# Performance work log

Hardware: AMD Instinct MI355X
Metric: run time of the kernel (lower is better)

Reference implementation:

```python
import math
import jax, jax.numpy as jnp
import numpy as np

L, D, H, DF, V, T, B = 4, 1024, 16, 4096, 32000, 2048, 1
HD = D // H
EPS = 1e-5

def _ln(x, w, b):
    m = jnp.mean(x, -1, keepdims=True)
    v = jnp.mean((x - m) ** 2, -1, keepdims=True)
    return (x - m) * jax.lax.rsqrt(v + EPS) * w + b

def setup_inputs() -> dict:
    key = jax.random.key(0)
    ks = jax.random.split(key, 8)
    s = 0.02
    return {
        'ids':   jax.random.randint(ks[0], (B, T), 0, V),
        'te':    jax.random.normal(ks[1], (V, D), jnp.float32) * s,
        'pe':    jax.random.normal(ks[2], (T, D), jnp.float32) * s,
        'qkv_w': jax.random.normal(ks[3], (L, D, 3 * D), jnp.float32) * s,
        'qkv_b': jnp.zeros((L, 3 * D), jnp.float32),
        'out_w': jax.random.normal(ks[4], (L, D, D), jnp.float32) * s,
        'out_b': jnp.zeros((L, D), jnp.float32),
        'ln1_w': jnp.ones((L, D), jnp.float32),
        'ln1_b': jnp.zeros((L, D), jnp.float32),
        'ln2_w': jnp.ones((L, D), jnp.float32),
        'ln2_b': jnp.zeros((L, D), jnp.float32),
        'up_w':  jax.random.normal(ks[5], (L, D, DF), jnp.float32) * s,
        'up_b':  jnp.zeros((L, DF), jnp.float32),
        'dn_w':  jax.random.normal(ks[6], (L, DF, D), jnp.float32) * s,
        'dn_b':  jnp.zeros((L, D), jnp.float32),
        'lnf_w': jnp.ones((D,), jnp.float32),
        'lnf_b': jnp.zeros((D,), jnp.float32),
    }

def reference(ids, te, pe, qkv_w, qkv_b, out_w, out_b, ln1_w, ln1_b,
              ln2_w, ln2_b, up_w, up_b, dn_w, dn_b, lnf_w, lnf_b):
    b, t = ids.shape
    x = te[ids] + pe[:t][None]                        # [b,t,D]
    causal = jnp.tril(jnp.ones((t, t), bool))          # [t,t]
    scale = 1.0 / math.sqrt(HD)
    for i in range(L):
        h = _ln(x, ln1_w[i], ln1_b[i])
        qkv = (h @ qkv_w[i] + qkv_b[i]).reshape(b, t, 3, H, HD)
        q, k, v = qkv[:, :, 0], qkv[:, :, 1], qkv[:, :, 2]
        sc = jnp.einsum('bqhd,bkhd->bhqk', q, k) * scale
        sc = jnp.where(causal, sc, -jnp.inf)
        att = jax.nn.softmax(sc, axis=-1)
        ao = jnp.einsum('bhqk,bkhd->bqhd', att, v).reshape(b, t, D)
        x = x + ao @ out_w[i] + out_b[i]
        h = _ln(x, ln2_w[i], ln2_b[i])
        x = x + jax.nn.silu(h @ up_w[i] + up_b[i]) @ dn_w[i] + dn_b[i]
    x = _ln(x, lnf_w, lnf_b)
    logits = x @ te.T                                  # tied head, no bias
    return logits
```

## Files before the change

### kernel.cpp

```cpp
#include <hip/hip_runtime.h>

typedef __attribute__((ext_vector_type(8))) short short8;
typedef __attribute__((ext_vector_type(4))) short short4v;
typedef __attribute__((ext_vector_type(4))) float f32x4;
typedef unsigned short u16;

#define Lc 4
#define Dc 1024
#define Hc 16
#define HDc 64
#define DFc 4096
#define Vc 32000
#define Tc 2048

__device__ __forceinline__ u16 f2bf(float f) {
  union { float f; unsigned u; } v; v.f = f;
  return (u16)((v.u + 0x7FFFu + ((v.u >> 16) & 1u)) >> 16);
}

__device__ __forceinline__ void gload_lds16(const u16* g, u16* l) {
  __builtin_amdgcn_global_load_lds(
      (const __attribute__((address_space(1))) unsigned int*)(g),
      (__attribute__((address_space(3))) unsigned int*)(l), 16, 0, 0);
}

#define BARS do { __builtin_amdgcn_s_barrier(); __builtin_amdgcn_sched_barrier(0); } while (0)
#define LGKM0 do { asm volatile("s_waitcnt lgkmcnt(0)" ::: "memory"); __builtin_amdgcn_sched_barrier(0); } while (0)
#define VMC(n) do { asm volatile("s_waitcnt vmcnt(" #n ")" ::: "memory"); __builtin_amdgcn_sched_barrier(0); } while (0)

__global__ __launch_bounds__(256) void castk(const float* __restrict__ in, u16* __restrict__ out) {
  size_t i = ((size_t)blockIdx.x * 256 + threadIdx.x) * 4;
  float4 v = *(const float4*)(in + i);
  short4v o; o[0] = f2bf(v.x); o[1] = f2bf(v.y); o[2] = f2bf(v.z); o[3] = f2bf(v.w);
  *(short4v*)(out + i) = o;
}

__global__ __launch_bounds__(256) void embedln(const int* __restrict__ ids, const float* __restrict__ te,
                                               const float* __restrict__ pe, const float* __restrict__ w,
                                               const float* __restrict__ b, float* __restrict__ x,
                                               u16* __restrict__ out) {
  int t = blockIdx.x, tid = threadIdx.x;
  int id = ids[t];
  float4 a = *(const float4*)(te + (size_t)id * Dc + tid * 4);
  float4 p = *(const float4*)(pe + (size_t)t * Dc + tid * 4);
  float4 v; v.x = a.x + p.x; v.y = a.y + p.y; v.z = a.z + p.z; v.w = a.w + p.w;
  size_t i = (size_t)t * Dc + tid * 4;
  *(float4*)(x + i) = v;
  float s = v.x + v.y + v.z + v.w;
  float q = v.x * v.x + v.y * v.y + v.z * v.z + v.w * v.w;
  #pragma unroll
  for (int off = 1; off < 64; off <<= 1) { s += __shfl_xor(s, off); q += __shfl_xor(q, off); }
  __shared__ float red[8];
  if ((tid & 63) == 0) { red[tid >> 6] = s; red[4 + (tid >> 6)] = q; }
  __syncthreads();
  s = red[0] + red[1] + red[2] + red[3];
  q = red[4] + red[5] + red[6] + red[7];
  float mean = s * (1.0f / Dc);
  float rstd = rsqrtf(q * (1.0f / Dc) - mean * mean + 1e-5f);
  float4 wv = *(const float4*)(w + tid * 4);
  float4 bv = *(const float4*)(b + tid * 4);
  out[i + 0] = f2bf((v.x - mean) * rstd * wv.x + bv.x);
  out[i + 1] = f2bf((v.y - mean) * rstd * wv.y + bv.y);
  out[i + 2] = f2bf((v.z - mean) * rstd * wv.z + bv.z);
  out[i + 3] = f2bf((v.w - mean) * rstd * wv.w + bv.w);
}

template<int SK>
__global__ __launch_bounds__(256) void combineln(float* __restrict__ x, const float* __restrict__ p,
                                                 const float* __restrict__ bias, const float* __restrict__ w,
                                                 const float* __restrict__ b, u16* __restrict__ out) {
  int t = blockIdx.x, tid = threadIdx.x;
  size_t i = (size_t)t * Dc + tid * 4;
  float4 v = *(const float4*)(x + i);
  #pragma unroll
  for (int s = 0; s < SK; s++) {
    float4 q2 = *(const float4*)(p + (size_t)s * Tc * Dc + i);
    v.x += q2.x; v.y += q2.y; v.z += q2.z; v.w += q2.w;
  }
  float4 bb = *(const float4*)(bias + tid * 4);
  v.x += bb.x; v.y += bb.y; v.z += bb.z; v.w += bb.w;
  *(float4*)(x + i) = v;
  float s = v.x + v.y + v.z + v.w;
  float q = v.x * v.x + v.y * v.y + v.z * v.z + v.w * v.w;
  #pragma unroll
  for (int off = 1; off < 64; off <<= 1) { s += __shfl_xor(s, off); q += __shfl_xor(q, off); }
  __shared__ float red[8];
  if ((tid & 63) == 0) { red[tid >> 6] = s; red[4 + (tid >> 6)] = q; }
  __syncthreads();
  s = red[0] + red[1] + red[2] + red[3];
  q = red[4] + red[5] + red[6] + red[7];
  float mean = s * (1.0f / Dc);
  float rstd = rsqrtf(q * (1.0f / Dc) - mean * mean + 1e-5f);
  float4 wv = *(const float4*)(w + tid * 4);
  float4 bv = *(const float4*)(b + tid * 4);
  out[i + 0] = f2bf((v.x - mean) * rstd * wv.x + bv.x);
  out[i + 1] = f2bf((v.y - mean) * rstd * wv.y + bv.y);
  out[i + 2] = f2bf((v.z - mean) * rstd * wv.z + bv.z);
  out[i + 3] = f2bf((v.w - mean) * rstd * wv.w + bv.w);
}

__global__ __launch_bounds__(256) void transpose4(const float* __restrict__ qw, const float* __restrict__ ow,
                                                  const float* __restrict__ uw, const float* __restrict__ dw,
                                                  u16* __restrict__ qT, u16* __restrict__ oT,
                                                  u16* __restrict__ uT, u16* __restrict__ dT) {
  __shared__ float tl[32][33];
  int id = blockIdx.x;
  const float* in; u16* out; int R, C, t;
  if (id < 3072)      { in = qw; out = qT; R = Dc;  C = 3 * Dc; t = id; }
  else if (id < 4096) { in = ow; out = oT; R = Dc;  C = Dc;     t = id - 3072; }
  else if (id < 8192) { in = uw; out = uT; R = Dc;  C = DFc;    t = id - 4096; }
  else                { in = dw; out = dT; R = DFc; C = Dc;     t = id - 8192; }
  int tilesX = C >> 5;
  int c0 = (t % tilesX) * 32, r0 = (t / tilesX) * 32;
  int lx = threadIdx.x & 31, ly = threadIdx.x >> 5;
  #pragma unroll
  for (int i = ly; i < 32; i += 8) tl[i][lx] = in[(size_t)(r0 + i) * C + c0 + lx];
  __syncthreads();
  #pragma unroll
  for (int i = ly; i < 32; i += 8) out[(size_t)(c0 + i) * R + r0 + lx] = f2bf(tl[lx][i]);
}

template<int EPI>
__global__ __launch_bounds__(256) void gemm128p(
    const u16* __restrict__ A, const u16* __restrict__ Bt, const float* __restrict__ bias,
    u16* __restrict__ outb, float* __restrict__ outf, int M, int N, int K, int KS) {
  __shared__ __align__(16) u16 lds[32768];
  u16* As = lds;
  u16* Bs = lds + 16384;
  const int NK = KS >> 6;

  int tid = threadIdx.x;
  int w = tid >> 6, lane = tid & 63;
  int lr = lane & 15, lg = lane >> 4;
  int wr = w >> 1, wc = w & 1;

  int m0 = blockIdx.y * 128, n0 = blockIdx.x * 128;
  int kbase = blockIdx.z * KS;

  int offg[4];
  #pragma unroll
  for (int j = 0; j < 4; j++) {
    int p = tid + j * 256;
    int row = p >> 3;
    int uc = (p & 7) ^ (row & 7);
    offg[j] = row * K + uc * 8;
  }
  const u16* aB = A + (size_t)m0 * K + kbase;
  const u16* bB = Bt + (size_t)n0 * K + kbase;

  auto stA = [&](int kt, int part) {
    u16* l = As + ((kt & 1) << 13) + w * 512;
    #pragma unroll
    for (int j = 2 * part; j < 2 * part + 2; j++)
      gload_lds16(aB + kt * 64 + offg[j], l + j * 2048);
  };
  auto stB = [&](int kt, int part) {
    u16* l = Bs + ((kt & 1) << 13) + w * 512;
    #pragma unroll
    for (int j = 2 * part; j < 2 * part + 2; j++)
      gload_lds16(bB + kt * 64 + offg[j], l + j * 2048);
  };

  int colx0 = ((0 * 4 + lg) ^ (lr & 7)) * 8;
  int colx1 = ((1 * 4 + lg) ^ (lr & 7)) * 8;
  int abase = (wr * 64 + lr) * 64;
  int bbase = (wc * 64 + lr) * 64;

  f32x4 acc[4][4] = {};

  stB(0, 0); stB(0, 1); stA(0, 0); stA(0, 1); stB(1, 0); stB(1, 1);
  VMC(4);
  BARS;

  for (int kt = 0; kt < NK; ++kt) {
    const u16* sA = As + ((kt & 1) << 13);
    const u16* sB = Bs + ((kt & 1) << 13);
    short8 af[4][2], bf[4][2];

    #pragma unroll
    for (int m = 0; m < 2; m++) {
      af[m][0] = *(const short8*)(sA + abase + m * 1024 + colx0);
      af[m][1] = *(const short8*)(sA + abase + m * 1024 + colx1);
      bf[m][0] = *(const short8*)(sB + bbase + m * 1024 + colx0);
      bf[m][1] = *(const short8*)(sB + bbase + m * 1024 + colx1);
    }
    if (kt + 1 < NK) stA(kt + 1, 0);
    BARS;
    LGKM0;
    __builtin_amdgcn_s_setprio(1);
    #pragma unroll
    for (int m = 0; m < 2; m++)
      #pragma unroll
      for (int n = 0; n < 2; n++)
        #pragma unroll
        for (int ks = 0; ks < 2; ks++)
          acc[m][n] = __builtin_amdgcn_mfma_f32_16x16x32_bf16(af[m][ks], bf[n][ks], acc[m][n], 0, 0, 0);
    __builtin_amdgcn_s_setprio(0);
    BARS;

    #pragma unroll
    for (int n = 2; n < 4; n++) {
      bf[n][0] = *(const short8*)(sB + bbase + n * 1024 + colx0);
      bf[n][1] = *(const short8*)(sB + bbase + n * 1024 + colx1);
    }
    if (kt + 1 < NK) stA(kt + 1, 1);
    BARS;
    LGKM0;
    __builtin_amdgcn_s_setprio(1);
    #pragma unroll
    for (int m = 0; m < 2; m++)
      #pragma unroll
      for (int n = 2; n < 4; n++)
        #pragma unroll
        for (int ks = 0; ks < 2; ks++)
          acc[m][n] = __builtin_amdgcn_mfma_f32_16x16x32_bf16(af[m][ks], bf[n][ks], acc[m][n], 0, 0, 0);
    __builtin_amdgcn_s_setprio(0);
    BARS;

    #pragma unroll
    for (int m = 2; m < 4; m++) {
      af[m][0] = *(const short8*)(sA + abase + m * 1024 + colx0);
      af[m][1] = *(const short8*)(sA + abase + m * 1024 + colx1);
    }
    if (kt + 2 < NK) stB(kt + 2, 0);
    BARS;
    LGKM0;
    __builtin_amdgcn_s_setprio(1);
    #pragma unroll
    for (int m = 2; m < 4; m++)
      #pragma unroll
      for (int n = 0; n < 2; n++)
        #pragma unroll
        for (int ks = 0; ks < 2; ks++)
          acc[m][n] = __builtin_amdgcn_mfma_f32_16x16x32_bf16(af[m][ks], bf[n][ks], acc[m][n], 0, 0, 0);
    __builtin_amdgcn_s_setprio(0);
    BARS;

    if (kt + 2 < NK) { stB(kt + 2, 1); VMC(4); }
    else if (kt + 1 < NK) { VMC(0); }
    BARS;
    __builtin_amdgcn_s_setprio(1);
    #pragma unroll
    for (int m = 2; m < 4; m++)
      #pragma unroll
      for (int n = 2; n < 4; n++)
        #pragma unroll
        for (int ks = 0; ks < 2; ks++)
          acc[m][n] = __builtin_amdgcn_mfma_f32_16x16x32_bf16(af[m][ks], bf[n][ks], acc[m][n], 0, 0, 0);
    __builtin_amdgcn_s_setprio(0);
    BARS;
  }

  float* op = outf + (EPI == 4 ? (size_t)blockIdx.z * M * N : 0);
  u16* vtp = (u16*)outf;
  #pragma unroll
  for (int n = 0; n < 4; n++) {
    int gn = n0 + wc * 64 + n * 16 + lr;
    float bv = (EPI == 0 || EPI == 1 || EPI == 5) ? bias[gn] : 0.0f;
    #pragma unroll
    for (int m = 0; m < 4; m++) {
      if (EPI == 5 && gn >= 2 * Dc) {
        int gmb = m0 + wr * 64 + m * 16 + lg * 4;
        short4v o;
        #pragma unroll
        for (int r = 0; r < 4; r++) o[r] = (short)f2bf(acc[m][n][r] + bv);
        *(short4v*)(vtp + (size_t)(gn - 2 * Dc) * Tc + gmb) = o;
      } else {
        #pragma unroll
        for (int r = 0; r < 4; r++) {
          int gm = m0 + wr * 64 + m * 16 + lg * 4 + r;
          float v = acc[m][n][r] + bv;
          size_t idx = (size_t)gm * N + gn;
          if (EPI == 0 || EPI == 5) outb[idx] = f2bf(v);
          else if (EPI == 1) outb[idx] = f2bf(v / (1.0f + __expf(-v)));
          else op[idx] = v;
        }
      }
    }
  }
}

__global__ __launch_bounds__(512) void gemm256(const u16* __restrict__ A, const u16* __restrict__ Bt,
                                               float* __restrict__ outf, int M, int N, int K) {
  __shared__ __align__(16) u16 lds[65536];
  u16* AsU = lds;
  u16* BsU = lds + 32768;
  const int NK = K >> 6;

  int tid = threadIdx.x;
  int w = tid >> 6, lane = tid & 63;
  int lr = lane & 15, lg = lane >> 4;
  int wr = w >> 2, wc = w & 3;

  int flat = blockIdx.y * gridDim.x + blockIdx.x;
  {
    int nwg = gridDim.x * gridDim.y;
    int q = nwg >> 3, r = nwg & 7, xc = flat & 7, s = flat >> 3;
    flat = (xc < r ? xc * (q + 1) : r * (q + 1) + (xc - r) * q) + s;
  }
  int bm = flat % gridDim.x, bn = flat / gridDim.x;
  int m0 = bm * 256, n0 = bn * 256;

  int row0 = tid >> 3;
  int uc0 = (tid & 7) ^ (row0 & 7);
  int offg = row0 * K + uc0 * 8;
  const u16* aB = A + (size_t)m0 * K;
  const u16* bB = Bt + (size_t)n0 * K;

  auto stA = [&](int kt, int half) {
    const u16* g = aB + (size_t)half * 128 * K + kt * 64 + offg;
    u16* l = AsU + (((kt & 1) * 2 + half) << 13) + w * 512;
    gload_lds16(g, l);
    gload_lds16(g + 64 * K, l + 4096);
  };
  auto stB = [&](int kt, int half) {
    const u16* g = bB + (size_t)half * 128 * K + kt * 64 + offg;
    u16* l = BsU + (((kt & 1) * 2 + half) << 13) + w * 512;
    gload_lds16(g, l);
    gload_lds16(g + 64 * K, l + 4096);
  };

  int colx0 = ((0 * 4 + lg) ^ (lr & 7)) * 8;
  int colx1 = ((1 * 4 + lg) ^ (lr & 7)) * 8;
  int arow = lr * 64;
  int brow = ((wc & 1) * 64 + lr) * 64;

  f32x4 acc[8][4] = {};

  stB(0, 0); stB(0, 1); stA(0, 0); stA(0, 1); stB(1, 0); stB(1, 1);
  VMC(4);
  BARS;

  for (int kt = 0; kt < NK; ++kt) {
    int slot = kt & 1;
    const u16* sA = AsU + ((slot * 2 + wr) << 13);
    const u16* sB = BsU + ((slot * 2 + (wc >> 1)) << 13);
    short8 af0[4][2], af1[4][2], bf0[2][2], bf1[2][2];

    #pragma unroll
    for (int m = 0; m < 4; m++) {
      af0[m][0] = *(const short8*)(sA + arow + m * 1024 + colx0);
      af0[m][1] = *(const short8*)(sA + arow + m * 1024 + colx1);
    }
    #pragma unroll
    for (int n = 0; n < 2; n++) {
      bf0[n][0] = *(const short8*)(sB + brow + n * 1024 + colx0);
      bf0[n][1] = *(const short8*)(sB + brow + n * 1024 + colx1);
    }
    if (kt + 1 < NK) stA(kt + 1, 0);
    BARS;
    LGKM0;
    __builtin_amdgcn_s_setprio(1);
    #pragma unroll
    for (int m = 0; m < 4; m++)
      #pragma unroll
      for (int n = 0; n < 2; n++)
        #pragma unroll
        for (int ks = 0; ks < 2; ks++)
          acc[m][n] = __builtin_amdgcn_mfma_f32_16x16x32_bf16(af0[m][ks], bf0[n][ks], acc[m][n], 0, 0, 0);
    __builtin_amdgcn_s_setprio(0);
    BARS;

    #pragma unroll
    for (int n = 0; n < 2; n++) {
      bf1[n][0] = *(const short8*)(sB + brow + (n + 2) * 1024 + colx0);
      bf1[n][1] = *(const short8*)(sB + brow + (n + 2) * 1024 + colx1);
    }
    if (kt + 1 < NK) stA(kt + 1, 1);
    BARS;
    LGKM0;
    __builtin_amdgcn_s_setprio(1);
    #pragma unroll
    for (int m = 0; m < 4; m++)
      #pragma unroll
      for (int n = 0; n < 2; n++)
        #pragma unroll
        for (int ks = 0; ks < 2; ks++)
          acc[m][n + 2] = __builtin_amdgcn_mfma_f32_16x16x32_bf16(af0[m][ks], bf1[n][ks], acc[m][n + 2], 0, 0, 0);
    __builtin_amdgcn_s_setprio(0);
    BARS;

    #pragma unroll
    for (int m = 0; m < 4; m++) {
      af1[m][0] = *(const short8*)(sA + arow + (m + 4) * 1024 + colx0);
      af1[m][1] = *(const short8*)(sA + arow + (m + 4) * 1024 + colx1);
    }
    if (kt + 2 < NK) stB(kt + 2, 0);
    BARS;
    LGKM0;
    __builtin_amdgcn_s_setprio(1);
    #pragma unroll
    for (int m = 0; m < 4; m++)
      #pragma unroll
      for (int n = 0; n < 2; n++)
        #pragma unroll
        for (int ks = 0; ks < 2; ks++)
          acc[m + 4][n] = __builtin_amdgcn_mfma_f32_16x16x32_bf16(af1[m][ks], bf0[n][ks], acc[m + 4][n], 0, 0, 0);
    __builtin_amdgcn_s_setprio(0);
    BARS;

    if (kt + 2 < NK) { stB(kt + 2, 1); VMC(4); }
    else if (kt + 1 < NK) { VMC(0); }
    BARS;
    __builtin_amdgcn_s_setprio(1);
    #pragma unroll
    for (int m = 0; m < 4; m++)
      #pragma unroll
      for (int n = 0; n < 2; n++)
        #pragma unroll
        for (int ks = 0; ks < 2; ks++)
          acc[m + 4][n + 2] = __builtin_amdgcn_mfma_f32_16x16x32_bf16(af1[m][ks], bf1[n][ks], acc[m + 4][n + 2], 0, 0, 0);
    __builtin_amdgcn_s_setprio(0);
    BARS;
  }

  #pragma unroll
  for (int m = 0; m < 8; m++) {
    #pragma unroll
    for (int n = 0; n < 4; n++) {
      int gn = n0 + wc * 64 + n * 16 + lr;
      #pragma unroll
      for (int r = 0; r < 4; r++) {
        int gm = m0 + wr * 128 + m * 16 + lg * 4 + r;
        outf[(size_t)gm * N + gn] = acc[m][n][r];
      }
    }
  }
}

__global__ __launch_bounds__(512) void attnk(const u16* __restrict__ qkv, const u16* __restrict__ vt,
                                             u16* __restrict__ ao) {
  __shared__ u16 Plds[8][16][72];
  __shared__ float Cacc[4][64][16];
  __shared__ float Cl[4][64][4];
  int hh = blockIdx.y, qb = blockIdx.x;
  int tid = threadIdx.x, l = tid & 63, w = tid >> 6;
  int w4 = w & 3, ishi = w >> 2;
  int lr = l & 15, lg = l >> 4;
  int qr0 = qb * 64 + w4 * 16;
  const u16* qbase = qkv + (size_t)(qr0 + lr) * (3 * Dc) + hh * HDc + lg * 8;
  short8 aq0 = *(const short8*)qbase;
  short8 aq1 = *(const short8*)(qbase + 32);
  f32x4 acco[4] = {};
  float rs[4] = {0.0f, 0.0f, 0.0f, 0.0f};
  int nkb = (qr0 + 79) >> 6;
  int half = nkb >> 1;
  int klo = ishi ? half : 0;
  int khi = ishi ? nkb : half;
  const float cl2 = 0.125f * 1.44269504088896f;
  for (int kb = klo; kb < khi; kb++) {
    int kk0 = kb * 64;
    float sv[4][4];
    bool msk = (kb == nkb - 1);
    #pragma unroll
    for (int st = 0; st < 4; st++) {
      int kt0 = kk0 + st * 16;
      const u16* kbase = qkv + (size_t)(kt0 + lr) * (3 * Dc) + Dc + hh * HDc + lg * 8;
      short8 bk0 = *(const short8*)kbase;
      short8 bk1 = *(const short8*)(kbase + 32);
      f32x4 s = {};
      s = __builtin_amdgcn_mfma_f32_16x16x32_bf16(aq0, bk0, s, 0, 0, 0);
      s = __builtin_amdgcn_mfma_f32_16x16x32_bf16(aq1, bk1, s, 0, 0, 0);
      if (msk) {
        int gcol = kt0 + lr;
        #pragma unroll
        for (int r = 0; r < 4; r++) {
          int grow = qr0 + lg * 4 + r;
          sv[st][r] = (gcol <= grow) ? s[r] * cl2 : -__builtin_inff();
        }
      } else {
        #pragma unroll
        for (int r = 0; r < 4; r++) sv[st][r] = s[r] * cl2;
      }
    }
    #pragma unroll
    for (int st = 0; st < 4; st++) {
      #pragma unroll
      for (int r = 0; r < 4; r++) {
        float p = __builtin_amdgcn_exp2f(fminf(sv[st][r], 45.0f));
        sv[st][r] = p;
        rs[r] += p;
      }
    }
    #pragma unroll
    for (int st = 0; st < 4; st++) {
      #pragma unroll
      for (int r = 0; r < 4; r++) Plds[w][lg * 4 + r][st * 16 + lr] = f2bf(sv[st][r]);
    }
    short8 pa0 = *(const short8*)&Plds[w][lr][lg * 8];
    short8 pa1 = *(const short8*)&Plds[w][lr][32 + lg * 8];
    #pragma unroll
    for (int nt = 0; nt < 4; nt++) {
      const u16* vbase = vt + (size_t)(hh * HDc + nt * 16 + lr) * Tc + kk0 + lg * 8;
      short8 bv0 = *(const short8*)vbase;
      short8 bv1 = *(const short8*)(vbase + 32);
      acco[nt] = __builtin_amdgcn_mfma_f32_16x16x32_bf16(pa0, bv0, acco[nt], 0, 0, 0);
      acco[nt] = __builtin_amdgcn_mfma_f32_16x16x32_bf16(pa1, bv1, acco[nt], 0, 0, 0);
    }
  }
  #pragma unroll
  for (int off = 1; off < 16; off <<= 1) {
    #pragma unroll
    for (int r = 0; r < 4; r++) rs[r] += __shfl_xor(rs[r], off);
  }
  if (ishi) {
    #pragma unroll
    for (int nt = 0; nt < 4; nt++)
      #pragma unroll
      for (int r = 0; r < 4; r++) Cacc[w4][l][nt * 4 + r] = acco[nt][r];
    #pragma unroll
    for (int r = 0; r < 4; r++) Cl[w4][l][r] = rs[r];
  }
  __syncthreads();
  if (!ishi) {
    float linv[4];
    #pragma unroll
    for (int r = 0; r < 4; r++) linv[r] = 1.0f / (rs[r] + Cl[w4][l][r]);
    #pragma unroll
    for (int nt = 0; nt < 4; nt++) {
      #pragma unroll
      for (int r = 0; r < 4; r++) {
        float val = (acco[nt][r] + Cacc[w4][l][nt * 4 + r]) * linv[r];
        ao[(size_t)(qr0 + lg * 4 + r) * Dc + hh * HDc + nt * 16 + lr] = f2bf(val);
      }
    }
  }
}

extern "C" void kernel_launch(void* const* d_in, const int* in_sizes, int n_in,
                              void* d_out, int out_size, void* d_ws, size_t ws_size,
                              hipStream_t stream) {
  const int*   ids   = (const int*)d_in[0];
  const float* te    = (const float*)d_in[1];
  const float* pe    = (const float*)d_in[2];
  const float* qkv_w = (const float*)d_in[3];
  const float* qkv_b = (const float*)d_in[4];
  const float* out_w = (const float*)d_in[5];
  const float* out_b = (const float*)d_in[6];
  const float* ln1_w = (const float*)d_in[7];
  const float* ln1_b = (const float*)d_in[8];
  const float* ln2_w = (const float*)d_in[9];
  const float* ln2_b = (const float*)d_in[10];
  const float* up_w  = (const float*)d_in[11];
  const float* up_b  = (const float*)d_in[12];
  const float* dn_w  = (const float*)d_in[13];
  const float* dn_b  = (const float*)d_in[14];
  const float* lnf_w = (const float*)d_in[15];
  const float* lnf_b = (const float*)d_in[16];
  float* logits = (float*)d_out;

  char* ws = (char*)d_ws;
  size_t off = 0;
  auto alloc = [&](size_t bytes) { void* p = ws + off; off += (bytes + 255) & ~(size_t)255; return p; };
  float* x    = (float*)alloc((size_t)Tc * Dc * 4);
  u16* hbuf   = (u16*)alloc((size_t)Tc * Dc * 2);
  u16* qkvb   = (u16*)alloc((size_t)Tc * 3 * Dc * 2);
  u16* aob    = (u16*)alloc((size_t)Tc * Dc * 2);
  u16* ubuf   = (u16*)alloc((size_t)Tc * DFc * 2);
  u16* vtb    = (u16*)alloc((size_t)Dc * Tc * 2);
  u16* tebf   = (u16*)alloc((size_t)Vc * Dc * 2);
  u16* qkvT   = (u16*)alloc((size_t)3 * Dc * Dc * 2);
  u16* outT   = (u16*)alloc((size_t)Dc * Dc * 2);
  u16* upT    = (u16*)alloc((size_t)DFc * Dc * 2);
  u16* dnT    = (u16*)alloc((size_t)Dc * DFc * 2);
  float* pbuf = (float*)alloc((size_t)4 * Tc * Dc * 4);

  castk<<<Vc * Dc / 1024, 256, 0, stream>>>(te, tebf);
  embedln<<<Tc, 256, 0, stream>>>(ids, te, pe, ln1_w, ln1_b, x, hbuf);

  for (int i = 0; i < Lc; i++) {
    transpose4<<<12288, 256, 0, stream>>>(
        qkv_w + (size_t)i * Dc * 3 * Dc, out_w + (size_t)i * Dc * Dc,
        up_w + (size_t)i * Dc * DFc, dn_w + (size_t)i * DFc * Dc,
        qkvT, outT, upT, dnT);

    gemm128p<5><<<dim3(3 * Dc / 128, Tc / 128, 1), 256, 0, stream>>>(
        hbuf, qkvT, qkv_b + (size_t)i * 3 * Dc, qkvb, (float*)vtb, Tc, 3 * Dc, Dc, Dc);
    attnk<<<dim3(Tc / 64, Hc), 512, 0, stream>>>(qkvb, vtb, aob);
    gemm128p<4><<<dim3(Dc / 128, Tc / 128, 2), 256, 0, stream>>>(
        aob, outT, nullptr, nullptr, pbuf, Tc, Dc, Dc, Dc / 2);
    combineln<2><<<Tc, 256, 0, stream>>>(x, pbuf, out_b + (size_t)i * Dc,
                                         ln2_w + (size_t)i * Dc, ln2_b + (size_t)i * Dc, hbuf);
    gemm128p<1><<<dim3(DFc / 128, Tc / 128, 1), 256, 0, stream>>>(
        hbuf, upT, up_b + (size_t)i * DFc, ubuf, nullptr, Tc, DFc, Dc, Dc);
    gemm128p<4><<<dim3(Dc / 128, Tc / 128, 4), 256, 0, stream>>>(
        ubuf, dnT, nullptr, nullptr, pbuf, Tc, Dc, DFc, DFc / 4);
    if (i < Lc - 1)
      combineln<4><<<Tc, 256, 0, stream>>>(x, pbuf, dn_b + (size_t)i * Dc,
                                           ln1_w + (size_t)(i + 1) * Dc, ln1_b + (size_t)(i + 1) * Dc, hbuf);
    else
      combineln<4><<<Tc, 256, 0, stream>>>(x, pbuf, dn_b + (size_t)i * Dc, lnf_w, lnf_b, hbuf);
  }

  gemm256<<<dim3(Tc / 256, Vc / 256), 512, 0, stream>>>(hbuf, tebf, logits, Tc, Vc, Dc);
}
```

Measured before the change: 1.141 ms.

## Shrink LM-head GEMM K-tile to 32 and reorder attention blocks for causal balance

The vocab-projection GEMM now uses a K step of 32 instead of 64. That halves its LDS footprint to 64 KB, which may let more workgroups share a CU. Each iteration issues one combined A/B stage and two MFMA phases with a new swizzle, replacing the four-phase split schedule. The attention grid is flattened to 1D with head-major ordering, and query-block order is reversed for half the heads so causal work is spread more evenly. In exchange the GEMM needs twice as many K iterations and barriers, which adds sync overhead per unit of MFMA work.

```diff
diff --git a/kernel.cpp b/kernel.cpp
--- a/kernel.cpp
+++ b/kernel.cpp
@@ -280,12 +280,12 @@
   }
 }
 
-__global__ __launch_bounds__(512) void gemm256(const u16* __restrict__ A, const u16* __restrict__ Bt,
-                                               float* __restrict__ outf, int M, int N, int K) {
-  __shared__ __align__(16) u16 lds[65536];
+__global__ __launch_bounds__(512) void gemm256b(const u16* __restrict__ A, const u16* __restrict__ Bt,
+                                                float* __restrict__ outf, int M, int N, int K) {
+  __shared__ __align__(16) u16 lds[32768];
   u16* AsU = lds;
-  u16* BsU = lds + 32768;
-  const int NK = K >> 6;
+  u16* BsU = lds + 16384;
+  const int NK = K >> 5;
 
   int tid = threadIdx.x;
   int w = tid >> 6, lane = tid & 63;
@@ -301,115 +301,66 @@
   int bm = flat % gridDim.x, bn = flat / gridDim.x;
   int m0 = bm * 256, n0 = bn * 256;
 
-  int row0 = tid >> 3;
-  int uc0 = (tid & 7) ^ (row0 & 7);
-  int offg = row0 * K + uc0 * 8;
+  int offg[2];
+  #pragma unroll
+  for (int j = 0; j < 2; j++) {
+    int p = tid + j * 512;
+    int row = p >> 2;
+    int uc = (p & 3) ^ ((row >> 1) & 3);
+    offg[j] = row * K + uc * 8;
+  }
   const u16* aB = A + (size_t)m0 * K;
   const u16* bB = Bt + (size_t)n0 * K;
 
-  auto stA = [&](int kt, int half) {
-    const u16* g = aB + (size_t)half * 128 * K + kt * 64 + offg;
-    u16* l = AsU + (((kt & 1) * 2 + half) << 13) + w * 512;
-    gload_lds16(g, l);
-    gload_lds16(g + 64 * K, l + 4096);
+  auto stage = [&](int kt) {
+    int so = (kt & 1) << 13;
+    u16* la = AsU + so + w * 512;
+    u16* lb = BsU + so + w * 512;
+    gload_lds16(aB + kt * 32 + offg[0], la);
+    gload_lds16(aB + kt * 32 + offg[1], la + 4096);
+    gload_lds16(bB + kt * 32 + offg[0], lb);
+    gload_lds16(bB + kt * 32 + offg[1], lb + 4096);
   };
-  auto stB = [&](int kt, int half) {
-    const u16* g = bB + (size_t)half * 128 * K + kt * 64 + offg;
-    u16* l = BsU + (((kt & 1) * 2 + half) << 13) + w * 512;
-    gload_lds16(g, l);
-    gload_lds16(g + 64 * K, l + 4096);
-  };
-
-  int colx0 = ((0 * 4 + lg) ^ (lr & 7)) * 8;
-  int colx1 = ((1 * 4 + lg) ^ (lr & 7)) * 8;
-  int arow = lr * 64;
-  int brow = ((wc & 1) * 64 + lr) * 64;
+
+  int colx = (lg ^ ((lr >> 1) & 3)) * 8;
+  int arow = (wr * 128 + lr) * 32;
+  int brow = (wc * 64 + lr) * 32;
 
   f32x4 acc[8][4] = {};
 
-  stB(0, 0); stB(0, 1); stA(0, 0); stA(0, 1); stB(1, 0); stB(1, 1);
+  stage(0); stage(1);
   VMC(4);
   BARS;
 
   for (int kt = 0; kt < NK; ++kt) {
-    int slot = kt & 1;
-    const u16* sA = AsU + ((slot * 2 + wr) << 13);
-    const u16* sB = BsU + ((slot * 2 + (wc >> 1)) << 13);
-    short8 af0[4][2], af1[4][2], bf0[2][2], bf1[2][2];
-
-    #pragma unroll
-    for (int m = 0; m < 4; m++) {
-      af0[m][0] = *(const short8*)(sA + arow + m * 1024 + colx0);
-      af0[m][1] = *(const short8*)(sA + arow + m * 1024 + colx1);
-    }
-    #pragma unroll
-    for (int n = 0; n < 2; n++) {
-      bf0[n][0] = *(const short8*)(sB + brow + n * 1024 + colx0);
-      bf0[n][1] = *(const short8*)(sB + brow + n * 1024 + colx1);
-    }
-    if (kt + 1 < NK) stA(kt + 1, 0);
+    const u16* sA = AsU + ((kt & 1) << 13);
+    const u16* sB = BsU + ((kt & 1) << 13);
+    short8 af[8], bf[4];
+
+    #pragma unroll
+    for (int m = 0; m < 8; m++) af[m] = *(const short8*)(sA + arow + m * 512 + colx);
+    #pragma unroll
+    for (int n = 0; n < 4; n++) bf[n] = *(const short8*)(sB + brow + n * 512 + colx);
     BARS;
     LGKM0;
     __builtin_amdgcn_s_setprio(1);
     #pragma unroll
-    for (int m = 0; m < 4; m++)
+    for (int m = 0; m < 8; m++)
       #pragma unroll
       for (int n = 0; n < 2; n++)
-        #pragma unroll
-        for (int ks = 0; ks < 2; ks++)
-          acc[m][n] = __builtin_amdgcn_mfma_f32_16x16x32_bf16(af0[m][ks], bf0[n][ks], acc[m][n], 0, 0, 0);
+        acc[m][n] = __builtin_amdgcn_mfma_f32_16x16x32_bf16(af[m], bf[n], acc[m][n], 0, 0, 0);
     __builtin_amdgcn_s_setprio(0);
     BARS;
 
-    #pragma unroll
-    for (int n = 0; n < 2; n++) {
-      bf1[n][0] = *(const short8*)(sB + brow + (n + 2) * 1024 + colx0);
-      bf1[n][1] = *(const short8*)(sB + brow + (n + 2) * 1024 + colx1);
-    }
-    if (kt + 1 < NK) stA(kt + 1, 1);
-    BARS;
-    LGKM0;
+    if (kt + 2 < NK) { stage(kt + 2); VMC(4); }
+    else if (kt + 1 < NK) { VMC(0); }
+    BARS;
     __builtin_amdgcn_s_setprio(1);
     #pragma unroll
-    for (int m = 0; m < 4; m++)
-      #pragma unroll
-      for (int n = 0; n < 2; n++)
-        #pragma unroll
-        for (int ks = 0; ks < 2; ks++)
-          acc[m][n + 2] = __builtin_amdgcn_mfma_f32_16x16x32_bf16(af0[m][ks], bf1[n][ks], acc[m][n + 2], 0, 0, 0);
-    __builtin_amdgcn_s_setprio(0);
-    BARS;
-
-    #pragma unroll
-    for (int m = 0; m < 4; m++) {
-      af1[m][0] = *(const short8*)(sA + arow + (m + 4) * 1024 + colx0);
-      af1[m][1] = *(const short8*)(sA + arow + (m + 4) * 1024 + colx1);
-    }
-    if (kt + 2 < NK) stB(kt + 2, 0);
-    BARS;
-    LGKM0;
-    __builtin_amdgcn_s_setprio(1);
-    #pragma unroll
-    for (int m = 0; m < 4; m++)
-      #pragma unroll
-      for (int n = 0; n < 2; n++)
-        #pragma unroll
-        for (int ks = 0; ks < 2; ks++)
-          acc[m + 4][n] = __builtin_amdgcn_mfma_f32_16x16x32_bf16(af1[m][ks], bf0[n][ks], acc[m + 4][n], 0, 0, 0);
-    __builtin_amdgcn_s_setprio(0);
-    BARS;
-
-    if (kt + 2 < NK) { stB(kt + 2, 1); VMC(4); }
-    else if (kt + 1 < NK) { VMC(0); }
-    BARS;
-    __builtin_amdgcn_s_setprio(1);
-    #pragma unroll
-    for (int m = 0; m < 4; m++)
-      #pragma unroll
-      for (int n = 0; n < 2; n++)
-        #pragma unroll
-        for (int ks = 0; ks < 2; ks++)
-          acc[m + 4][n + 2] = __builtin_amdgcn_mfma_f32_16x16x32_bf16(af1[m][ks], bf1[n][ks], acc[m + 4][n + 2], 0, 0, 0);
+    for (int m = 0; m < 8; m++)
+      #pragma unroll
+      for (int n = 2; n < 4; n++)
+        acc[m][n] = __builtin_amdgcn_mfma_f32_16x16x32_bf16(af[m], bf[n], acc[m][n], 0, 0, 0);
     __builtin_amdgcn_s_setprio(0);
     BARS;
   }
@@ -433,7 +384,9 @@
   __shared__ u16 Plds[8][16][72];
   __shared__ float Cacc[4][64][16];
   __shared__ float Cl[4][64][4];
-  int hh = blockIdx.y, qb = blockIdx.x;
+  int bid = blockIdx.x;
+  int hh = bid >> 5;
+  int qb = (bid & 256) ? (31 - (bid & 31)) : (bid & 31);
   int tid = threadIdx.x, l = tid & 63, w = tid >> 6;
   int w4 = w & 3, ishi = w >> 2;
   int lr = l & 15, lg = l >> 4;
@@ -576,7 +529,7 @@
 
     gemm128p<5><<<dim3(3 * Dc / 128, Tc / 128, 1), 256, 0, stream>>>(
         hbuf, qkvT, qkv_b + (size_t)i * 3 * Dc, qkvb, (float*)vtb, Tc, 3 * Dc, Dc, Dc);
-    attnk<<<dim3(Tc / 64, Hc), 512, 0, stream>>>(qkvb, vtb, aob);
+    attnk<<<512, 512, 0, stream>>>(qkvb, vtb, aob);
     gemm128p<4><<<dim3(Dc / 128, Tc / 128, 2), 256, 0, stream>>>(
         aob, outT, nullptr, nullptr, pbuf, Tc, Dc, Dc, Dc / 2);
     combineln<2><<<Tc, 256, 0, stream>>>(x, pbuf, out_b + (size_t)i * Dc,
@@ -592,5 +545,5 @@
       combineln<4><<<Tc, 256, 0, stream>>>(x, pbuf, dn_b + (size_t)i * Dc, lnf_w, lnf_b, hbuf);
   }
 
-  gemm256<<<dim3(Tc / 256, Vc / 256), 512, 0, stream>>>(hbuf, tebf, logits, Tc, Vc, Dc);
-}
+  gemm256b<<<dim3(Tc / 256, Vc / 256), 512, 0, stream>>>(hbuf, tebf, logits, Tc, Vc, Dc);
+}
```

Measured after the change: 959.9 us. 15.9% less time.

## Halve GEMM K-tile for higher occupancy and remap attention blocks for causal balance

Applied to the files above, without the earlier changes.

The 128x128 bf16 GEMM now uses a 32-wide K tile instead of 64. That halves its LDS use to 32 KB and requests 4 blocks per CU through launch_bounds. The old four-phase interleaved load/MFMA loop becomes a simpler double-buffered loop: it loads all fragments, syncs, prefetches tile kt+2, then issues 16 MFMAs. The attention kernel moves to a 1D grid and reverses query-block order for heads 8-15, so short and long causal blocks mix in dispatch order. The risks are twice as many barriers per unit of K work and less latency hiding inside each block, which the extra occupancy must make up for.

```diff
diff --git a/kernel.cpp b/kernel.cpp
--- a/kernel.cpp
+++ b/kernel.cpp
@@ -121,13 +121,13 @@
 }
 
 template<int EPI>
-__global__ __launch_bounds__(256) void gemm128p(
+__global__ __launch_bounds__(256, 4) void gemm128c(
     const u16* __restrict__ A, const u16* __restrict__ Bt, const float* __restrict__ bias,
     u16* __restrict__ outb, float* __restrict__ outf, int M, int N, int K, int KS) {
-  __shared__ __align__(16) u16 lds[32768];
+  __shared__ __align__(16) u16 lds[16384];
   u16* As = lds;
-  u16* Bs = lds + 16384;
-  const int NK = KS >> 6;
+  u16* Bs = lds + 8192;
+  const int NK = KS >> 5;
 
   int tid = threadIdx.x;
   int w = tid >> 6, lane = tid & 63;
@@ -137,117 +137,57 @@
   int m0 = blockIdx.y * 128, n0 = blockIdx.x * 128;
   int kbase = blockIdx.z * KS;
 
-  int offg[4];
-  #pragma unroll
-  for (int j = 0; j < 4; j++) {
+  int offg[2];
+  #pragma unroll
+  for (int j = 0; j < 2; j++) {
     int p = tid + j * 256;
-    int row = p >> 3;
-    int uc = (p & 7) ^ (row & 7);
+    int row = p >> 2;
+    int uc = (p & 3) ^ ((row >> 1) & 3);
     offg[j] = row * K + uc * 8;
   }
   const u16* aB = A + (size_t)m0 * K + kbase;
   const u16* bB = Bt + (size_t)n0 * K + kbase;
 
-  auto stA = [&](int kt, int part) {
-    u16* l = As + ((kt & 1) << 13) + w * 512;
-    #pragma unroll
-    for (int j = 2 * part; j < 2 * part + 2; j++)
-      gload_lds16(aB + kt * 64 + offg[j], l + j * 2048);
+  auto stage = [&](int kt) {
+    int so = (kt & 1) << 12;
+    u16* la = As + so + w * 512;
+    u16* lb = Bs + so + w * 512;
+    gload_lds16(aB + kt * 32 + offg[0], la);
+    gload_lds16(aB + kt * 32 + offg[1], la + 2048);
+    gload_lds16(bB + kt * 32 + offg[0], lb);
+    gload_lds16(bB + kt * 32 + offg[1], lb + 2048);
   };
-  auto stB = [&](int kt, int part) {
-    u16* l = Bs + ((kt & 1) << 13) + w * 512;
-    #pragma unroll
-    for (int j = 2 * part; j < 2 * part + 2; j++)
-      gload_lds16(bB + kt * 64 + offg[j], l + j * 2048);
-  };
-
-  int colx0 = ((0 * 4 + lg) ^ (lr & 7)) * 8;
-  int colx1 = ((1 * 4 + lg) ^ (lr & 7)) * 8;
-  int abase = (wr * 64 + lr) * 64;
-  int bbase = (wc * 64 + lr) * 64;
+
+  int colx = (lg ^ ((lr >> 1) & 3)) * 8;
+  int abase = (wr * 64 + lr) * 32;
+  int bbase = (wc * 64 + lr) * 32;
 
   f32x4 acc[4][4] = {};
 
-  stB(0, 0); stB(0, 1); stA(0, 0); stA(0, 1); stB(1, 0); stB(1, 1);
+  stage(0); stage(1);
   VMC(4);
   BARS;
 
   for (int kt = 0; kt < NK; ++kt) {
-    const u16* sA = As + ((kt & 1) << 13);
-    const u16* sB = Bs + ((kt & 1) << 13);
-    short8 af[4][2], bf[4][2];
-
-    #pragma unroll
-    for (int m = 0; m < 2; m++) {
-      af[m][0] = *(const short8*)(sA + abase + m * 1024 + colx0);
-      af[m][1] = *(const short8*)(sA + abase + m * 1024 + colx1);
-      bf[m][0] = *(const short8*)(sB + bbase + m * 1024 + colx0);
-      bf[m][1] = *(const short8*)(sB + bbase + m * 1024 + colx1);
-    }
-    if (kt + 1 < NK) stA(kt + 1, 0);
-    BARS;
+    const u16* sA = As + ((kt & 1) << 12);
+    const u16* sB = Bs + ((kt & 1) << 12);
+    short8 af[4], bf[4];
+    #pragma unroll
+    for (int m = 0; m < 4; m++) af[m] = *(const short8*)(sA + abase + m * 512 + colx);
+    #pragma unroll
+    for (int n = 0; n < 4; n++) bf[n] = *(const short8*)(sB + bbase + n * 512 + colx);
     LGKM0;
+    BARS;
+    if (kt + 2 < NK) stage(kt + 2);
     __builtin_amdgcn_s_setprio(1);
     #pragma unroll
-    for (int m = 0; m < 2; m++)
-      #pragma unroll
-      for (int n = 0; n < 2; n++)
-        #pragma unroll
-        for (int ks = 0; ks < 2; ks++)
-          acc[m][n] = __builtin_amdgcn_mfma_f32_16x16x32_bf16(af[m][ks], bf[n][ks], acc[m][n], 0, 0, 0);
+    for (int m = 0; m < 4; m++)
+      #pragma unroll
+      for (int n = 0; n < 4; n++)
+        acc[m][n] = __builtin_amdgcn_mfma_f32_16x16x32_bf16(af[m], bf[n], acc[m][n], 0, 0, 0);
     __builtin_amdgcn_s_setprio(0);
-    BARS;
-
-    #pragma unroll
-    for (int n = 2; n < 4; n++) {
-      bf[n][0] = *(const short8*)(sB + bbase + n * 1024 + colx0);
-      bf[n][1] = *(const short8*)(sB + bbase + n * 1024 + colx1);
-    }
-    if (kt + 1 < NK) stA(kt + 1, 1);
-    BARS;
-    LGKM0;
-    __builtin_amdgcn_s_setprio(1);
-    #pragma unroll
-    for (int m = 0; m < 2; m++)
-      #pragma unroll
-      for (int n = 2; n < 4; n++)
-        #pragma unroll
-        for (int ks = 0; ks < 2; ks++)
-          acc[m][n] = __builtin_amdgcn_mfma_f32_16x16x32_bf16(af[m][ks], bf[n][ks], acc[m][n], 0, 0, 0);
-    __builtin_amdgcn_s_setprio(0);
-    BARS;
-
-    #pragma unroll
-    for (int m = 2; m < 4; m++) {
-      af[m][0] = *(const short8*)(sA + abase + m * 1024 + colx0);
-      af[m][1] = *(const short8*)(sA + abase + m * 1024 + colx1);
-    }
-    if (kt + 2 < NK) stB(kt + 2, 0);
-    BARS;
-    LGKM0;
-    __builtin_amdgcn_s_setprio(1);
-    #pragma unroll
-    for (int m = 2; m < 4; m++)
-      #pragma unroll
-      for (int n = 0; n < 2; n++)
-        #pragma unroll
-        for (int ks = 0; ks < 2; ks++)
-          acc[m][n] = __builtin_amdgcn_mfma_f32_16x16x32_bf16(af[m][ks], bf[n][ks], acc[m][n], 0, 0, 0);
-    __builtin_amdgcn_s_setprio(0);
-    BARS;
-
-    if (kt + 2 < NK) { stB(kt + 2, 1); VMC(4); }
+    if (kt + 2 < NK) { VMC(4); }
     else if (kt + 1 < NK) { VMC(0); }
-    BARS;
-    __builtin_amdgcn_s_setprio(1);
-    #pragma unroll
-    for (int m = 2; m < 4; m++)
-      #pragma unroll
-      for (int n = 2; n < 4; n++)
-        #pragma unroll
-        for (int ks = 0; ks < 2; ks++)
-          acc[m][n] = __builtin_amdgcn_mfma_f32_16x16x32_bf16(af[m][ks], bf[n][ks], acc[m][n], 0, 0, 0);
-    __builtin_amdgcn_s_setprio(0);
     BARS;
   }
 
@@ -433,7 +373,9 @@
   __shared__ u16 Plds[8][16][72];
   __shared__ float Cacc[4][64][16];
   __shared__ float Cl[4][64][4];
-  int hh = blockIdx.y, qb = blockIdx.x;
+  int bid = blockIdx.x;
+  int hh = bid >> 5;
+  int qb = (bid & 256) ? (31 - (bid & 31)) : (bid & 31);
   int tid = threadIdx.x, l = tid & 63, w = tid >> 6;
   int w4 = w & 3, ishi = w >> 2;
   int lr = l & 15, lg = l >> 4;
@@ -574,16 +516,16 @@
         up_w + (size_t)i * Dc * DFc, dn_w + (size_t)i * DFc * Dc,
         qkvT, outT, upT, dnT);
 
-    gemm128p<5><<<dim3(3 * Dc / 128, Tc / 128, 1), 256, 0, stream>>>(
+    gemm128c<5><<<dim3(3 * Dc / 128, Tc / 128, 1), 256, 0, stream>>>(
         hbuf, qkvT, qkv_b + (size_t)i * 3 * Dc, qkvb, (float*)vtb, Tc, 3 * Dc, Dc, Dc);
-    attnk<<<dim3(Tc / 64, Hc), 512, 0, stream>>>(qkvb, vtb, aob);
-    gemm128p<4><<<dim3(Dc / 128, Tc / 128, 2), 256, 0, stream>>>(
+    attnk<<<512, 512, 0, stream>>>(qkvb, vtb, aob);
+    gemm128c<4><<<dim3(Dc / 128, Tc / 128, 2), 256, 0, stream>>>(
         aob, outT, nullptr, nullptr, pbuf, Tc, Dc, Dc, Dc / 2);
     combineln<2><<<Tc, 256, 0, stream>>>(x, pbuf, out_b + (size_t)i * Dc,
                                          ln2_w + (size_t)i * Dc, ln2_b + (size_t)i * Dc, hbuf);
-    gemm128p<1><<<dim3(DFc / 128, Tc / 128, 1), 256, 0, stream>>>(
+    gemm128c<1><<<dim3(DFc / 128, Tc / 128, 1), 256, 0, stream>>>(
         hbuf, upT, up_b + (size_t)i * DFc, ubuf, nullptr, Tc, DFc, Dc, Dc);
-    gemm128p<4><<<dim3(Dc / 128, Tc / 128, 4), 256, 0, stream>>>(
+    gemm128c<4><<<dim3(Dc / 128, Tc / 128, 4), 256, 0, stream>>>(
         ubuf, dnT, nullptr, nullptr, pbuf, Tc, Dc, DFc, DFc / 4);
     if (i < Lc - 1)
       combineln<4><<<Tc, 256, 0, stream>>>(x, pbuf, dn_b + (size_t)i * Dc,
```

After: 969.3 us. -15.0%, faster.

## Merge GEMM k-loop phases into two halves and reorder attention blocks

Applied to the files above, without the earlier changes.

Both GEMM kernels drop from four sub-phases per k-tile to two. Global-to-LDS prefetches are issued in larger batches, and all B fragments are loaded up front, which cuts barriers and setprio toggles per iteration. The cost is more live registers and less interleaving of loads with MFMA work. The attention launch becomes a 1D grid of 512 blocks. The query-block order is reversed for the upper half of heads, so heavy causal blocks spread more evenly across CUs.

```diff
diff --git a/kernel.cpp b/kernel.cpp
--- a/kernel.cpp
+++ b/kernel.cpp
@@ -121,7 +121,7 @@
 }
 
 template<int EPI>
-__global__ __launch_bounds__(256) void gemm128p(
+__global__ __launch_bounds__(256) void gemm128m(
     const u16* __restrict__ A, const u16* __restrict__ Bt, const float* __restrict__ bias,
     u16* __restrict__ outb, float* __restrict__ outf, int M, int N, int K, int KS) {
   __shared__ __align__(16) u16 lds[32768];
@@ -148,16 +148,16 @@
   const u16* aB = A + (size_t)m0 * K + kbase;
   const u16* bB = Bt + (size_t)n0 * K + kbase;
 
-  auto stA = [&](int kt, int part) {
+  auto stA = [&](int kt) {
     u16* l = As + ((kt & 1) << 13) + w * 512;
     #pragma unroll
-    for (int j = 2 * part; j < 2 * part + 2; j++)
+    for (int j = 0; j < 4; j++)
       gload_lds16(aB + kt * 64 + offg[j], l + j * 2048);
   };
-  auto stB = [&](int kt, int part) {
+  auto stB = [&](int kt) {
     u16* l = Bs + ((kt & 1) << 13) + w * 512;
     #pragma unroll
-    for (int j = 2 * part; j < 2 * part + 2; j++)
+    for (int j = 0; j < 4; j++)
       gload_lds16(bB + kt * 64 + offg[j], l + j * 2048);
   };
 
@@ -168,7 +168,7 @@
 
   f32x4 acc[4][4] = {};
 
-  stB(0, 0); stB(0, 1); stA(0, 0); stA(0, 1); stB(1, 0); stB(1, 1);
+  stB(0); stA(0); stB(1);
   VMC(4);
   BARS;
 
@@ -181,17 +181,20 @@
     for (int m = 0; m < 2; m++) {
       af[m][0] = *(const short8*)(sA + abase + m * 1024 + colx0);
       af[m][1] = *(const short8*)(sA + abase + m * 1024 + colx1);
-      bf[m][0] = *(const short8*)(sB + bbase + m * 1024 + colx0);
-      bf[m][1] = *(const short8*)(sB + bbase + m * 1024 + colx1);
-    }
-    if (kt + 1 < NK) stA(kt + 1, 0);
+    }
+    #pragma unroll
+    for (int n = 0; n < 4; n++) {
+      bf[n][0] = *(const short8*)(sB + bbase + n * 1024 + colx0);
+      bf[n][1] = *(const short8*)(sB + bbase + n * 1024 + colx1);
+    }
+    if (kt + 1 < NK) stA(kt + 1);
     BARS;
     LGKM0;
     __builtin_amdgcn_s_setprio(1);
     #pragma unroll
     for (int m = 0; m < 2; m++)
       #pragma unroll
-      for (int n = 0; n < 2; n++)
+      for (int n = 0; n < 4; n++)
         #pragma unroll
         for (int ks = 0; ks < 2; ks++)
           acc[m][n] = __builtin_amdgcn_mfma_f32_16x16x32_bf16(af[m][ks], bf[n][ks], acc[m][n], 0, 0, 0);
@@ -199,51 +202,19 @@
     BARS;
 
     #pragma unroll
-    for (int n = 2; n < 4; n++) {
-      bf[n][0] = *(const short8*)(sB + bbase + n * 1024 + colx0);
-      bf[n][1] = *(const short8*)(sB + bbase + n * 1024 + colx1);
-    }
-    if (kt + 1 < NK) stA(kt + 1, 1);
-    BARS;
-    LGKM0;
-    __builtin_amdgcn_s_setprio(1);
-    #pragma unroll
-    for (int m = 0; m < 2; m++)
-      #pragma unroll
-      for (int n = 2; n < 4; n++)
-        #pragma unroll
-        for (int ks = 0; ks < 2; ks++)
-          acc[m][n] = __builtin_amdgcn_mfma_f32_16x16x32_bf16(af[m][ks], bf[n][ks], acc[m][n], 0, 0, 0);
-    __builtin_amdgcn_s_setprio(0);
-    BARS;
-
-    #pragma unroll
     for (int m = 2; m < 4; m++) {
       af[m][0] = *(const short8*)(sA + abase + m * 1024 + colx0);
       af[m][1] = *(const short8*)(sA + abase + m * 1024 + colx1);
     }
-    if (kt + 2 < NK) stB(kt + 2, 0);
+    if (kt + 2 < NK) { stB(kt + 2); VMC(4); }
+    else if (kt + 1 < NK) { VMC(0); }
     BARS;
     LGKM0;
     __builtin_amdgcn_s_setprio(1);
     #pragma unroll
     for (int m = 2; m < 4; m++)
       #pragma unroll
-      for (int n = 0; n < 2; n++)
-        #pragma unroll
-        for (int ks = 0; ks < 2; ks++)
-          acc[m][n] = __builtin_amdgcn_mfma_f32_16x16x32_bf16(af[m][ks], bf[n][ks], acc[m][n], 0, 0, 0);
-    __builtin_amdgcn_s_setprio(0);
-    BARS;
-
-    if (kt + 2 < NK) { stB(kt + 2, 1); VMC(4); }
-    else if (kt + 1 < NK) { VMC(0); }
-    BARS;
-    __builtin_amdgcn_s_setprio(1);
-    #pragma unroll
-    for (int m = 2; m < 4; m++)
-      #pragma unroll
-      for (int n = 2; n < 4; n++)
+      for (int n = 0; n < 4; n++)
         #pragma unroll
         for (int ks = 0; ks < 2; ks++)
           acc[m][n] = __builtin_amdgcn_mfma_f32_16x16x32_bf16(af[m][ks], bf[n][ks], acc[m][n], 0, 0, 0);
@@ -346,8 +317,10 @@
     for (int n = 0; n < 2; n++) {
       bf0[n][0] = *(const short8*)(sB + brow + n * 1024 + colx0);
       bf0[n][1] = *(const short8*)(sB + brow + n * 1024 + colx1);
-    }
-    if (kt + 1 < NK) stA(kt + 1, 0);
+      bf1[n][0] = *(const short8*)(sB + brow + (n + 2) * 1024 + colx0);
+      bf1[n][1] = *(const short8*)(sB + brow + (n + 2) * 1024 + colx1);
+    }
+    if (kt + 1 < NK) { stA(kt + 1, 0); stA(kt + 1, 1); }
     BARS;
     LGKM0;
     __builtin_amdgcn_s_setprio(1);
@@ -358,18 +331,6 @@
         #pragma unroll
         for (int ks = 0; ks < 2; ks++)
           acc[m][n] = __builtin_amdgcn_mfma_f32_16x16x32_bf16(af0[m][ks], bf0[n][ks], acc[m][n], 0, 0, 0);
-    __builtin_amdgcn_s_setprio(0);
-    BARS;
-
-    #pragma unroll
-    for (int n = 0; n < 2; n++) {
-      bf1[n][0] = *(const short8*)(sB + brow + (n + 2) * 1024 + colx0);
-      bf1[n][1] = *(const short8*)(sB + brow + (n + 2) * 1024 + colx1);
-    }
-    if (kt + 1 < NK) stA(kt + 1, 1);
-    BARS;
-    LGKM0;
-    __builtin_amdgcn_s_setprio(1);
     #pragma unroll
     for (int m = 0; m < 4; m++)
       #pragma unroll
@@ -385,7 +346,8 @@
       af1[m][0] = *(const short8*)(sA + arow + (m + 4) * 1024 + colx0);
       af1[m][1] = *(const short8*)(sA + arow + (m + 4) * 1024 + colx1);
     }
-    if (kt + 2 < NK) stB(kt + 2, 0);
+    if (kt + 2 < NK) { stB(kt + 2, 0); stB(kt + 2, 1); VMC(4); }
+    else if (kt + 1 < NK) { VMC(0); }
     BARS;
     LGKM0;
     __builtin_amdgcn_s_setprio(1);
@@ -396,13 +358,6 @@
         #pragma unroll
         for (int ks = 0; ks < 2; ks++)
           acc[m + 4][n] = __builtin_amdgcn_mfma_f32_16x16x32_bf16(af1[m][ks], bf0[n][ks], acc[m + 4][n], 0, 0, 0);
-    __builtin_amdgcn_s_setprio(0);
-    BARS;
-
-    if (kt + 2 < NK) { stB(kt + 2, 1); VMC(4); }
-    else if (kt + 1 < NK) { VMC(0); }
-    BARS;
-    __builtin_amdgcn_s_setprio(1);
     #pragma unroll
     for (int m = 0; m < 4; m++)
       #pragma unroll
@@ -433,7 +388,9 @@
   __shared__ u16 Plds[8][16][72];
   __shared__ float Cacc[4][64][16];
   __shared__ float Cl[4][64][4];
-  int hh = blockIdx.y, qb = blockIdx.x;
+  int bid = blockIdx.x;
+  int hh = bid >> 5;
+  int qb = (bid & 256) ? (31 - (bid & 31)) : (bid & 31);
   int tid = threadIdx.x, l = tid & 63, w = tid >> 6;
   int w4 = w & 3, ishi = w >> 2;
   int lr = l & 15, lg = l >> 4;
@@ -574,16 +531,16 @@
         up_w + (size_t)i * Dc * DFc, dn_w + (size_t)i * DFc * Dc,
         qkvT, outT, upT, dnT);
 
-    gemm128p<5><<<dim3(3 * Dc / 128, Tc / 128, 1), 256, 0, stream>>>(
+    gemm128m<5><<<dim3(3 * Dc / 128, Tc / 128, 1), 256, 0, stream>>>(
         hbuf, qkvT, qkv_b + (size_t)i * 3 * Dc, qkvb, (float*)vtb, Tc, 3 * Dc, Dc, Dc);
-    attnk<<<dim3(Tc / 64, Hc), 512, 0, stream>>>(qkvb, vtb, aob);
-    gemm128p<4><<<dim3(Dc / 128, Tc / 128, 2), 256, 0, stream>>>(
+    attnk<<<512, 512, 0, stream>>>(qkvb, vtb, aob);
+    gemm128m<4><<<dim3(Dc / 128, Tc / 128, 2), 256, 0, stream>>>(
         aob, outT, nullptr, nullptr, pbuf, Tc, Dc, Dc, Dc / 2);
     combineln<2><<<Tc, 256, 0, stream>>>(x, pbuf, out_b + (size_t)i * Dc,
                                          ln2_w + (size_t)i * Dc, ln2_b + (size_t)i * Dc, hbuf);
-    gemm128p<1><<<dim3(DFc / 128, Tc / 128, 1), 256, 0, stream>>>(
+    gemm128m<1><<<dim3(DFc / 128, Tc / 128, 1), 256, 0, stream>>>(
         hbuf, upT, up_b + (size_t)i * DFc, ubuf, nullptr, Tc, DFc, Dc, Dc);
-    gemm128p<4><<<dim3(Dc / 128, Tc / 128, 4), 256, 0, stream>>>(
+    gemm128m<4><<<dim3(Dc / 128, Tc / 128, 4), 256, 0, stream>>>(
         ubuf, dnT, nullptr, nullptr, pbuf, Tc, Dc, DFc, DFc / 4);
     if (i < Lc - 1)
       combineln<4><<<Tc, 256, 0, stream>>>(x, pbuf, dn_b + (size_t)i * Dc,
```

Measured after the change: 938.7 us. 1.22x faster.
